# Kernel optimization log

Measured on AMD Instinct MI355X. Metric: run time of the kernel, lower is better.

## Reference

```python
import jax, jax.numpy as jnp
import numpy as np

T, HQ, HKV, D, R = 2048, 16, 4, 128, 8
NEG = -1e30


def apply_rope(x, cos, sin):
    # x: [T, H, D]; cos/sin: [T, D//2]; non-interleaved rotary over full head dim
    c = jnp.concatenate([cos, cos], axis=-1)[:, None, :]  # [T,1,D]
    s = jnp.concatenate([sin, sin], axis=-1)[:, None, :]
    half = x.shape[-1] // 2
    x1, x2 = x[..., :half], x[..., half:]
    rot = jnp.concatenate([-x2, x1], axis=-1)
    return x * c + rot * s


def setup_inputs() -> dict:
    key = jax.random.key(0)
    kq, kk, kv = jax.random.split(key, 3)
    q = jax.random.normal(kq, (T, HQ, D), dtype=jnp.float32)
    k = jax.random.normal(kk, (T, HKV, D), dtype=jnp.float32)
    v = jax.random.normal(kv, (T, HKV, D), dtype=jnp.float32)
    # standard rotary tables
    inv_freq = 1.0 / (10000.0 ** (np.arange(0, D, 2, dtype=np.float32) / D))
    ang = np.arange(T, dtype=np.float32)[:, None] * inv_freq[None, :]  # [T, D/2]
    cos = jnp.asarray(np.cos(ang), dtype=jnp.float32)
    sin = jnp.asarray(np.sin(ang), dtype=jnp.float32)
    # block-causal ranges: q block r attends to keys [0, (r+1)*B)
    B = T // R
    q_ranges = jnp.asarray([[r * B, (r + 1) * B] for r in range(R)], dtype=jnp.int32)
    k_ranges = jnp.asarray([[0, (r + 1) * B] for r in range(R)], dtype=jnp.int32)
    return {"q": q, "k": k, "v": v, "cos": cos, "sin": sin,
            "q_ranges": q_ranges, "k_ranges": k_ranges}


def reference(q, k, v, cos, sin, q_ranges, k_ranges):
    scale = 1.0 / jnp.sqrt(jnp.float32(D))
    qh = apply_rope(q, cos, sin)
    kh = apply_rope(k, cos, sin)
    rep = HQ // HKV
    kr = jnp.repeat(kh, rep, axis=1)  # [T,HQ,D]
    vr = jnp.repeat(v, rep, axis=1)
    idx = jnp.arange(T)
    qm = (idx[None, :] >= q_ranges[:, :1]) & (idx[None, :] < q_ranges[:, 1:])  # [R,T]
    km = (idx[None, :] >= k_ranges[:, :1]) & (idx[None, :] < k_ranges[:, 1:])  # [R,T]
    mask = jnp.any(qm[:, :, None] & km[:, None, :], axis=0)  # [T,T] union over ranges
    scores = jnp.einsum('qhd,khd->hqk', qh, kr) * scale  # [HQ,T,T]
    scores = jnp.where(mask[None], scores, NEG)
    p = jax.nn.softmax(scores, axis=-1)
    row_valid = jnp.any(mask, axis=-1)  # [T]
    p = jnp.where(row_valid[None, :, None], p, 0.0)  # uncovered q rows output zero
    out = jnp.einsum('hqk,khd->qhd', p, vr)
    return out
```

## Files before the change

### kernel.cpp

```cpp
#include <hip/hip_runtime.h>
#include <hip/hip_bf16.h>

#define T_   2048
#define HQ_  16
#define HKV_ 4
#define D_   128
#define QBLK 64
#define NQB  (T_/QBLK)
#define KVBLK 64

typedef float f32x4 __attribute__((ext_vector_type(4)));
typedef __bf16 bf16x8 __attribute__((ext_vector_type(8)));
typedef unsigned short u16;
typedef unsigned short u16x8 __attribute__((ext_vector_type(8)));
typedef unsigned long long u64;

__device__ __forceinline__ u16 f2bf(float f) {
  unsigned u = __builtin_bit_cast(unsigned, f);
  u += 0x7FFFu + ((u >> 16) & 1u);
  return (u16)(u >> 16);
}

#define QK_BLOCKS 1280
__global__ __launch_bounds__(256) void prep_all(
    const float* __restrict__ q, const float* __restrict__ k,
    const float* __restrict__ v, const float* __restrict__ ct,
    const float* __restrict__ st,
    u16* __restrict__ qr, u16* __restrict__ kr, u16* __restrict__ vt)
{
  __shared__ __attribute__((aligned(16))) char Lv[32 * 144];
  const int tid = threadIdx.x;
  const int bid = blockIdx.x;
  if (bid < QK_BLOCKS) {
    const float scale = 0.08838834764831845f;
    const int NQT = T_ * HQ_ * 8;
    int gid = bid * 256 + tid;
    if (gid < NQT) {
      int j0 = (gid & 7) * 8;
      int h  = (gid >> 3) & 15;
      int t  = gid >> 7;
      const float* base = q + ((size_t)t * HQ_ + h) * D_;
      const float* cb = ct + t * 64 + j0;
      const float* sb = st + t * 64 + j0;
      u16 lo[8], hi[8];
#pragma unroll
      for (int e = 0; e < 8; ++e) {
        float x1 = base[j0 + e], x2 = base[j0 + 64 + e];
        float c = cb[e], s = sb[e];
        lo[e] = f2bf((x1 * c - x2 * s) * scale);
        hi[e] = f2bf((x2 * c + x1 * s) * scale);
      }
      u16* orow = qr + ((size_t)h * T_ + t) * D_;
      *reinterpret_cast<u16x8*>(orow + j0)      = *reinterpret_cast<u16x8*>(lo);
      *reinterpret_cast<u16x8*>(orow + 64 + j0) = *reinterpret_cast<u16x8*>(hi);
    } else {
      int th = gid - NQT;
      int j0 = (th & 7) * 8;
      int hh = (th >> 3) & 3;
      int t  = th >> 5;
      const float* base = k + ((size_t)t * HKV_ + hh) * D_;
      const float* cb = ct + t * 64 + j0;
      const float* sb = st + t * 64 + j0;
      u16 lo[8], hi[8];
#pragma unroll
      for (int e = 0; e < 8; ++e) {
        float x1 = base[j0 + e], x2 = base[j0 + 64 + e];
        float c = cb[e], s = sb[e];
        lo[e] = f2bf(x1 * c - x2 * s);
        hi[e] = f2bf(x2 * c + x1 * s);
      }
      u16* orow = kr + ((size_t)hh * T_ + t) * D_;
      *reinterpret_cast<u16x8*>(orow + j0)      = *reinterpret_cast<u16x8*>(lo);
      *reinterpret_cast<u16x8*>(orow + 64 + j0) = *reinterpret_cast<u16x8*>(hi);
    }
  } else {
    int vbid = bid - QK_BLOCKS;
    int hh = vbid & 3;
    int t0 = ((vbid >> 2) & 31) * 64;
    int d0 = (vbid >> 7) * 32;
    {
      int r  = tid >> 2;
      int dg = tid & 3;
      const float* vrow = v + ((size_t)(t0 + r) * HKV_ + hh) * D_ + d0 + dg * 8;
      float4 f0 = *reinterpret_cast<const float4*>(vrow);
      float4 f1 = *reinterpret_cast<const float4*>(vrow + 4);
      float fv[8] = {f0.x, f0.y, f0.z, f0.w, f1.x, f1.y, f1.z, f1.w};
#pragma unroll
      for (int e = 0; e < 8; ++e)
        *reinterpret_cast<u16*>(Lv + (dg * 8 + e) * 144 + r * 2) = f2bf(fv[e]);
    }
    __syncthreads();
    {
      int dl = tid >> 3;
      int c0 = (tid & 7) * 16;
      u16x8 val = *reinterpret_cast<const u16x8*>(Lv + dl * 144 + c0);
      u16* orow = vt + ((size_t)(hh * D_ + d0 + dl)) * T_ + t0 + (c0 >> 1);
      *reinterpret_cast<u16x8*>(orow) = val;
    }
  }
}

__global__ __launch_bounds__(256, 2) void attn_fwd(
    const u16* __restrict__ qr, const u16* __restrict__ kr,
    const u16* __restrict__ vt, float* __restrict__ out)
{
  __shared__ __attribute__((aligned(16))) char lds[73728];

  const int tid  = threadIdx.x;
  const int lane = tid & 63;
  const int wv   = tid >> 6;
  char* Plds = lds + 65536 + wv * 2048;

  const int bid = blockIdx.x;
  const int qb  = (NQB - 1) - (bid >> 4);
  const int h   = bid & 15;
  const int hkv = h >> 2;
  const int q0  = qb * QBLK + wv * 16;
  const int nt  = ((qb >> 2) + 1) * 4;

  const int lm = lane & 15;
  const int lh = lane >> 4;

  bf16x8 qf[4];
  {
    const u16* qrow = qr + ((size_t)h * T_ + q0 + lm) * D_;
#pragma unroll
    for (int kb = 0; kb < 4; ++kb)
      qf[kb] = *reinterpret_cast<const bf16x8*>(qrow + kb * 32 + lh * 8);
  }

  const u16* kbase = kr + (size_t)hkv * T_ * D_;
  const u16* vbase = vt + (size_t)hkv * D_ * T_;

  bf16x8 kpf[4], vpf[4];
#pragma unroll
  for (int j = 0; j < 4; ++j) {
    kpf[j] = *reinterpret_cast<const bf16x8*>(kbase + j * 2048 + tid * 8);
    int d = j * 32 + (tid >> 3);
    vpf[j] = *reinterpret_cast<const bf16x8*>(vbase + (size_t)d * T_ + (tid & 7) * 8);
  }

  f32x4 accO[8];
#pragma unroll
  for (int c = 0; c < 8; ++c) accO[c] = (f32x4){0.f, 0.f, 0.f, 0.f};
  float mrun = -1e30f, lrun = 0.f;

  for (int t = 0; t < nt; ++t) {
    char* Klds  = lds + (t & 1) * 16384;
    char* VTlds = lds + 32768 + (t & 1) * 16384;
#pragma unroll
    for (int j = 0; j < 4; ++j) {
      int off = j * 4096 + tid * 16;
      int row = off >> 8;
      *reinterpret_cast<bf16x8*>(Klds + (off ^ ((row & 7) << 4))) = kpf[j];
      int d = j * 32 + (tid >> 3);
      int offv = d * 128 + (tid & 7) * 16;
      *reinterpret_cast<bf16x8*>(VTlds + (offv ^ ((d & 7) << 4))) = vpf[j];
    }
    if (t + 1 < nt) {
      const u16* kb2 = kbase + (size_t)(t + 1) * KVBLK * D_;
      const u16* vb2 = vbase + (size_t)(t + 1) * KVBLK;
#pragma unroll
      for (int j = 0; j < 4; ++j) {
        kpf[j] = *reinterpret_cast<const bf16x8*>(kb2 + j * 2048 + tid * 8);
        int d = j * 32 + (tid >> 3);
        vpf[j] = *reinterpret_cast<const bf16x8*>(vb2 + (size_t)d * T_ + (tid & 7) * 8);
      }
    }
    __syncthreads();

    f32x4 s[4];
#pragma unroll
    for (int g = 0; g < 4; ++g) s[g] = (f32x4){0.f, 0.f, 0.f, 0.f};
    __builtin_amdgcn_s_setprio(1);
#pragma unroll
    for (int kb = 0; kb < 4; ++kb) {
#pragma unroll
      for (int g = 0; g < 4; ++g) {
        int row = lm + 16 * g;
        bf16x8 kf = *reinterpret_cast<const bf16x8*>(
            Klds + ((row * 256 + kb * 64 + lh * 16) ^ ((row & 7) << 4)));
        s[g] = __builtin_amdgcn_mfma_f32_16x16x32_bf16(kf, qf[kb], s[g], 0, 0, 0);
      }
    }
    __builtin_amdgcn_s_setprio(0);

    float tmax = -1e30f;
#pragma unroll
    for (int g = 0; g < 4; ++g)
      tmax = fmaxf(tmax, fmaxf(fmaxf(s[g][0], s[g][1]), fmaxf(s[g][2], s[g][3])));
    tmax = fmaxf(tmax, __shfl_xor(tmax, 16));
    tmax = fmaxf(tmax, __shfl_xor(tmax, 32));
    float mnew  = fmaxf(mrun, tmax);
    float alpha = __expf(mrun - mnew);
    float psum = 0.f;
#pragma unroll
    for (int g = 0; g < 4; ++g) {
      float p0 = __expf(s[g][0] - mnew), p1 = __expf(s[g][1] - mnew);
      float p2 = __expf(s[g][2] - mnew), p3 = __expf(s[g][3] - mnew);
      psum += (p0 + p1) + (p2 + p3);
      u64 w = (u64)f2bf(p0) | ((u64)f2bf(p1) << 16) |
              ((u64)f2bf(p2) << 32) | ((u64)f2bf(p3) << 48);
      *reinterpret_cast<u64*>(
          Plds + lm * 128 + ((g * 32 + lh * 8) ^ ((lm & 7) << 4))) = w;
    }
    psum += __shfl_xor(psum, 16);
    psum += __shfl_xor(psum, 32);
    lrun = lrun * alpha + psum;
    mrun = mnew;
#pragma unroll
    for (int c = 0; c < 8; ++c) {
      accO[c][0] *= alpha; accO[c][1] *= alpha;
      accO[c][2] *= alpha; accO[c][3] *= alpha;
    }

    bf16x8 pf[2];
#pragma unroll
    for (int half = 0; half < 2; ++half)
      pf[half] = *reinterpret_cast<const bf16x8*>(
          Plds + lm * 128 + ((half * 64 + lh * 16) ^ ((lm & 7) << 4)));
    __builtin_amdgcn_s_setprio(1);
#pragma unroll
    for (int c = 0; c < 8; ++c) {
#pragma unroll
      for (int half = 0; half < 2; ++half) {
        int row = c * 16 + lm;
        bf16x8 vf = *reinterpret_cast<const bf16x8*>(
            VTlds + ((row * 128 + half * 64 + lh * 16) ^ ((row & 7) << 4)));
        accO[c] = __builtin_amdgcn_mfma_f32_16x16x32_bf16(vf, pf[half], accO[c], 0, 0, 0);
      }
    }
    __builtin_amdgcn_s_setprio(0);
  }

  float inv = 1.f / lrun;
  float* orow = out + ((size_t)(q0 + lm) * HQ_ + h) * D_ + lh * 4;
#pragma unroll
  for (int c = 0; c < 8; ++c) {
    f32x4 o;
    o[0] = accO[c][0] * inv; o[1] = accO[c][1] * inv;
    o[2] = accO[c][2] * inv; o[3] = accO[c][3] * inv;
    *reinterpret_cast<f32x4*>(orow + c * 16) = o;
  }
}

extern "C" void kernel_launch(void* const* d_in, const int* in_sizes, int n_in,
                              void* d_out, int out_size, void* d_ws, size_t ws_size,
                              hipStream_t stream) {
  const float* q  = (const float*)d_in[0];
  const float* k  = (const float*)d_in[1];
  const float* v  = (const float*)d_in[2];
  const float* ct = (const float*)d_in[3];
  const float* st = (const float*)d_in[4];

  u16* qr = (u16*)d_ws;
  u16* kr = qr + (size_t)T_ * HQ_ * D_;
  u16* vt = kr + (size_t)T_ * HKV_ * D_;
  float* out = (float*)d_out;

  prep_all<<<QK_BLOCKS + 512, 256, 0, stream>>>(q, k, v, ct, st, qr, kr, vt);
  attn_fwd<<<NQB * HQ_, 256, 0, stream>>>(qr, kr, vt, out);
}
```

Baseline: 133.0 us.

## Software-pipeline PV MFMA into next iteration, remap block schedule, use packed bf16 convert

Defers each tile's P·V MFMAs to the start of the next iteration, issuing them alongside the Q·K MFMAs so softmax work can overlap matrix-core work. The V fragments are held in 16 registers across iterations. The block-to-(head, q-block) mapping is changed to interleave long and short causal q-blocks, aiming for better load balance across CUs. The manual bf16 rounding is replaced with the v_cvt_pk_bf16_f32 instruction. The extra live registers risk spills or lower occupancy under the 2-block launch bound.

```diff
diff --git a/kernel.cpp b/kernel.cpp
--- a/kernel.cpp
+++ b/kernel.cpp
@@ -14,6 +14,7 @@
 typedef unsigned short u16;
 typedef unsigned short u16x8 __attribute__((ext_vector_type(8)));
 typedef unsigned long long u64;
+typedef unsigned u32;
 
 __device__ __forceinline__ u16 f2bf(float f) {
   unsigned u = __builtin_bit_cast(unsigned, f);
@@ -112,8 +113,10 @@
   char* Plds = lds + 65536 + wv * 2048;
 
   const int bid = blockIdx.x;
-  const int qb  = (NQB - 1) - (bid >> 4);
-  const int h   = bid & 15;
+  const int f   = (bid ^ (bid >> 8)) & 1;
+  const int x   = (bid >> 4) & 15;
+  const int h   = ((bid >> 1) & 7) | (((bid >> 8) & 1) << 3);
+  const int qb  = f ? (31 - x) : x;
   const int hkv = h >> 2;
   const int q0  = qb * QBLK + wv * 16;
   const int nt  = ((qb >> 2) + 1) * 4;
@@ -132,18 +135,28 @@
   const u16* kbase = kr + (size_t)hkv * T_ * D_;
   const u16* vbase = vt + (size_t)hkv * D_ * T_;
 
-  bf16x8 kpf[4], vpf[4];
+  bf16x8 ksta[4], vsta[4];
 #pragma unroll
   for (int j = 0; j < 4; ++j) {
-    kpf[j] = *reinterpret_cast<const bf16x8*>(kbase + j * 2048 + tid * 8);
+    ksta[j] = *reinterpret_cast<const bf16x8*>(kbase + j * 2048 + tid * 8);
     int d = j * 32 + (tid >> 3);
-    vpf[j] = *reinterpret_cast<const bf16x8*>(vbase + (size_t)d * T_ + (tid & 7) * 8);
+    vsta[j] = *reinterpret_cast<const bf16x8*>(vbase + (size_t)d * T_ + (tid & 7) * 8);
   }
 
   f32x4 accO[8];
 #pragma unroll
   for (int c = 0; c < 8; ++c) accO[c] = (f32x4){0.f, 0.f, 0.f, 0.f};
   float mrun = -1e30f, lrun = 0.f;
+
+  bf16x8 vf[16], pf[2];
+#pragma unroll
+  for (int i = 0; i < 16; ++i)
+#pragma unroll
+    for (int e = 0; e < 8; ++e) vf[i][e] = (__bf16)0.f;
+#pragma unroll
+  for (int i = 0; i < 2; ++i)
+#pragma unroll
+    for (int e = 0; e < 8; ++e) pf[i][e] = (__bf16)0.f;
 
   for (int t = 0; t < nt; ++t) {
     char* Klds  = lds + (t & 1) * 16384;
@@ -152,19 +165,19 @@
     for (int j = 0; j < 4; ++j) {
       int off = j * 4096 + tid * 16;
       int row = off >> 8;
-      *reinterpret_cast<bf16x8*>(Klds + (off ^ ((row & 7) << 4))) = kpf[j];
+      *reinterpret_cast<bf16x8*>(Klds + (off ^ ((row & 7) << 4))) = ksta[j];
       int d = j * 32 + (tid >> 3);
       int offv = d * 128 + (tid & 7) * 16;
-      *reinterpret_cast<bf16x8*>(VTlds + (offv ^ ((d & 7) << 4))) = vpf[j];
+      *reinterpret_cast<bf16x8*>(VTlds + (offv ^ ((d & 7) << 4))) = vsta[j];
     }
     if (t + 1 < nt) {
       const u16* kb2 = kbase + (size_t)(t + 1) * KVBLK * D_;
       const u16* vb2 = vbase + (size_t)(t + 1) * KVBLK;
 #pragma unroll
       for (int j = 0; j < 4; ++j) {
-        kpf[j] = *reinterpret_cast<const bf16x8*>(kb2 + j * 2048 + tid * 8);
+        ksta[j] = *reinterpret_cast<const bf16x8*>(kb2 + j * 2048 + tid * 8);
         int d = j * 32 + (tid >> 3);
-        vpf[j] = *reinterpret_cast<const bf16x8*>(vb2 + (size_t)d * T_ + (tid & 7) * 8);
+        vsta[j] = *reinterpret_cast<const bf16x8*>(vb2 + (size_t)d * T_ + (tid & 7) * 8);
       }
     }
     __syncthreads();
@@ -173,6 +186,11 @@
 #pragma unroll
     for (int g = 0; g < 4; ++g) s[g] = (f32x4){0.f, 0.f, 0.f, 0.f};
     __builtin_amdgcn_s_setprio(1);
+#pragma unroll
+    for (int c = 0; c < 8; ++c) {
+      accO[c] = __builtin_amdgcn_mfma_f32_16x16x32_bf16(vf[2*c],   pf[0], accO[c], 0, 0, 0);
+      accO[c] = __builtin_amdgcn_mfma_f32_16x16x32_bf16(vf[2*c+1], pf[1], accO[c], 0, 0, 0);
+    }
 #pragma unroll
     for (int kb = 0; kb < 4; ++kb) {
 #pragma unroll
@@ -184,6 +202,15 @@
       }
     }
     __builtin_amdgcn_s_setprio(0);
+
+#pragma unroll
+    for (int c = 0; c < 8; ++c)
+#pragma unroll
+      for (int half = 0; half < 2; ++half) {
+        int row = c * 16 + lm;
+        vf[2*c + half] = *reinterpret_cast<const bf16x8*>(
+            VTlds + ((row * 128 + half * 64 + lh * 16) ^ ((row & 7) << 4)));
+      }
 
     float tmax = -1e30f;
 #pragma unroll
@@ -199,8 +226,10 @@
       float p0 = __expf(s[g][0] - mnew), p1 = __expf(s[g][1] - mnew);
       float p2 = __expf(s[g][2] - mnew), p3 = __expf(s[g][3] - mnew);
       psum += (p0 + p1) + (p2 + p3);
-      u64 w = (u64)f2bf(p0) | ((u64)f2bf(p1) << 16) |
-              ((u64)f2bf(p2) << 32) | ((u64)f2bf(p3) << 48);
+      u32 r01, r23;
+      asm("v_cvt_pk_bf16_f32 %0, %1, %2" : "=v"(r01) : "v"(p0), "v"(p1));
+      asm("v_cvt_pk_bf16_f32 %0, %1, %2" : "=v"(r23) : "v"(p2), "v"(p3));
+      u64 w = (u64)r01 | ((u64)r23 << 32);
       *reinterpret_cast<u64*>(
           Plds + lm * 128 + ((g * 32 + lh * 8) ^ ((lm & 7) << 4))) = w;
     }
@@ -213,25 +242,19 @@
       accO[c][0] *= alpha; accO[c][1] *= alpha;
       accO[c][2] *= alpha; accO[c][3] *= alpha;
     }
-
-    bf16x8 pf[2];
 #pragma unroll
     for (int half = 0; half < 2; ++half)
       pf[half] = *reinterpret_cast<const bf16x8*>(
           Plds + lm * 128 + ((half * 64 + lh * 16) ^ ((lm & 7) << 4)));
-    __builtin_amdgcn_s_setprio(1);
-#pragma unroll
-    for (int c = 0; c < 8; ++c) {
-#pragma unroll
-      for (int half = 0; half < 2; ++half) {
-        int row = c * 16 + lm;
-        bf16x8 vf = *reinterpret_cast<const bf16x8*>(
-            VTlds + ((row * 128 + half * 64 + lh * 16) ^ ((row & 7) << 4)));
-        accO[c] = __builtin_amdgcn_mfma_f32_16x16x32_bf16(vf, pf[half], accO[c], 0, 0, 0);
-      }
-    }
-    __builtin_amdgcn_s_setprio(0);
-  }
+  }
+
+  __builtin_amdgcn_s_setprio(1);
+#pragma unroll
+  for (int c = 0; c < 8; ++c) {
+    accO[c] = __builtin_amdgcn_mfma_f32_16x16x32_bf16(vf[2*c],   pf[0], accO[c], 0, 0, 0);
+    accO[c] = __builtin_amdgcn_mfma_f32_16x16x32_bf16(vf[2*c+1], pf[1], accO[c], 0, 0, 0);
+  }
+  __builtin_amdgcn_s_setprio(0);
 
   float inv = 1.f / lrun;
   float* orow = out + ((size_t)(q0 + lm) * HQ_ + h) * D_ + lh * 4;
```

Result: faster. 129.8 us (-2.4%).

## Halve KV tile to raise occupancy, remap blocks, use packed bf16 convert

Applied to the files above, without the earlier changes.

Shrinks the KV tile from 64 to 32 keys, which cuts LDS from 72KB to 40KB and lets launch bounds request 4 blocks per CU instead of 2. The V-transpose LDS layout is repacked so two d-rows share a 128-byte row with an XOR swizzle. Block-to-(head, q-block) mapping is changed to interleave long and short causal rows and balance the load. The softmax probabilities are packed with the v_cvt_pk_bf16_f32 instruction. In exchange it doubles the loop trip count, so there are twice as many barriers and softmax reductions per key processed.

```diff
diff --git a/kernel.cpp b/kernel.cpp
--- a/kernel.cpp
+++ b/kernel.cpp
@@ -7,13 +7,14 @@
 #define D_   128
 #define QBLK 64
 #define NQB  (T_/QBLK)
-#define KVBLK 64
+#define KVBLK 32
 
 typedef float f32x4 __attribute__((ext_vector_type(4)));
 typedef __bf16 bf16x8 __attribute__((ext_vector_type(8)));
 typedef unsigned short u16;
 typedef unsigned short u16x8 __attribute__((ext_vector_type(8)));
 typedef unsigned long long u64;
+typedef unsigned u32;
 
 __device__ __forceinline__ u16 f2bf(float f) {
   unsigned u = __builtin_bit_cast(unsigned, f);
@@ -100,23 +101,25 @@
   }
 }
 
-__global__ __launch_bounds__(256, 2) void attn_fwd(
+__global__ __launch_bounds__(256, 4) void attn_fwd(
     const u16* __restrict__ qr, const u16* __restrict__ kr,
     const u16* __restrict__ vt, float* __restrict__ out)
 {
-  __shared__ __attribute__((aligned(16))) char lds[73728];
+  __shared__ __attribute__((aligned(16))) char lds[40960];
 
   const int tid  = threadIdx.x;
   const int lane = tid & 63;
   const int wv   = tid >> 6;
-  char* Plds = lds + 65536 + wv * 2048;
+  char* Plds = lds + 32768 + wv * 2048;
 
   const int bid = blockIdx.x;
-  const int qb  = (NQB - 1) - (bid >> 4);
-  const int h   = bid & 15;
+  const int f   = (bid ^ (bid >> 8)) & 1;
+  const int x   = (bid >> 4) & 15;
+  const int h   = ((bid >> 1) & 7) | (((bid >> 8) & 1) << 3);
+  const int qb  = f ? (31 - x) : x;
   const int hkv = h >> 2;
   const int q0  = qb * QBLK + wv * 16;
-  const int nt  = ((qb >> 2) + 1) * 4;
+  const int nt  = ((qb >> 2) + 1) * 8;
 
   const int lm = lane & 15;
   const int lh = lane >> 4;
@@ -132,12 +135,18 @@
   const u16* kbase = kr + (size_t)hkv * T_ * D_;
   const u16* vbase = vt + (size_t)hkv * D_ * T_;
 
-  bf16x8 kpf[4], vpf[4];
-#pragma unroll
-  for (int j = 0; j < 4; ++j) {
-    kpf[j] = *reinterpret_cast<const bf16x8*>(kbase + j * 2048 + tid * 8);
-    int d = j * 32 + (tid >> 3);
-    vpf[j] = *reinterpret_cast<const bf16x8*>(vbase + (size_t)d * T_ + (tid & 7) * 8);
+  const int ks_row  = tid >> 4;
+  const int ks_colb = (tid & 15) * 16;
+  const int vs_d    = tid >> 1;
+  const int vs_half = tid & 1;
+
+  bf16x8 ksta[2], vsta[2];
+#pragma unroll
+  for (int j = 0; j < 2; ++j) {
+    ksta[j] = *reinterpret_cast<const bf16x8*>(
+        kbase + (size_t)(ks_row + j * 16) * D_ + (ks_colb >> 1));
+    vsta[j] = *reinterpret_cast<const bf16x8*>(
+        vbase + (size_t)vs_d * T_ + vs_half * 16 + j * 8);
   }
 
   f32x4 accO[8];
@@ -146,37 +155,38 @@
   float mrun = -1e30f, lrun = 0.f;
 
   for (int t = 0; t < nt; ++t) {
-    char* Klds  = lds + (t & 1) * 16384;
-    char* VTlds = lds + 32768 + (t & 1) * 16384;
-#pragma unroll
-    for (int j = 0; j < 4; ++j) {
-      int off = j * 4096 + tid * 16;
-      int row = off >> 8;
-      *reinterpret_cast<bf16x8*>(Klds + (off ^ ((row & 7) << 4))) = kpf[j];
-      int d = j * 32 + (tid >> 3);
-      int offv = d * 128 + (tid & 7) * 16;
-      *reinterpret_cast<bf16x8*>(VTlds + (offv ^ ((d & 7) << 4))) = vpf[j];
+    char* Klds  = lds + (t & 1) * 8192;
+    char* VTlds = lds + 16384 + (t & 1) * 8192;
+#pragma unroll
+    for (int j = 0; j < 2; ++j) {
+      int row = ks_row + j * 16;
+      int off = row * 256 + ks_colb;
+      *reinterpret_cast<bf16x8*>(Klds + (off ^ ((row & 7) << 4))) = ksta[j];
+      int prow = vs_d >> 1;
+      int colb = (vs_d & 1) * 64 + vs_half * 32 + j * 16;
+      *reinterpret_cast<bf16x8*>(
+          VTlds + prow * 128 + (colb ^ ((prow & 7) << 4))) = vsta[j];
     }
     if (t + 1 < nt) {
-      const u16* kb2 = kbase + (size_t)(t + 1) * KVBLK * D_;
-      const u16* vb2 = vbase + (size_t)(t + 1) * KVBLK;
-#pragma unroll
-      for (int j = 0; j < 4; ++j) {
-        kpf[j] = *reinterpret_cast<const bf16x8*>(kb2 + j * 2048 + tid * 8);
-        int d = j * 32 + (tid >> 3);
-        vpf[j] = *reinterpret_cast<const bf16x8*>(vb2 + (size_t)d * T_ + (tid & 7) * 8);
+      const int kv1 = (t + 1) * KVBLK;
+#pragma unroll
+      for (int j = 0; j < 2; ++j) {
+        ksta[j] = *reinterpret_cast<const bf16x8*>(
+            kbase + (size_t)(kv1 + ks_row + j * 16) * D_ + (ks_colb >> 1));
+        vsta[j] = *reinterpret_cast<const bf16x8*>(
+            vbase + (size_t)vs_d * T_ + kv1 + vs_half * 16 + j * 8);
       }
     }
     __syncthreads();
 
-    f32x4 s[4];
-#pragma unroll
-    for (int g = 0; g < 4; ++g) s[g] = (f32x4){0.f, 0.f, 0.f, 0.f};
+    f32x4 s[2];
+#pragma unroll
+    for (int g = 0; g < 2; ++g) s[g] = (f32x4){0.f, 0.f, 0.f, 0.f};
     __builtin_amdgcn_s_setprio(1);
 #pragma unroll
     for (int kb = 0; kb < 4; ++kb) {
 #pragma unroll
-      for (int g = 0; g < 4; ++g) {
+      for (int g = 0; g < 2; ++g) {
         int row = lm + 16 * g;
         bf16x8 kf = *reinterpret_cast<const bf16x8*>(
             Klds + ((row * 256 + kb * 64 + lh * 16) ^ ((row & 7) << 4)));
@@ -185,22 +195,22 @@
     }
     __builtin_amdgcn_s_setprio(0);
 
-    float tmax = -1e30f;
-#pragma unroll
-    for (int g = 0; g < 4; ++g)
-      tmax = fmaxf(tmax, fmaxf(fmaxf(s[g][0], s[g][1]), fmaxf(s[g][2], s[g][3])));
+    float tmax = fmaxf(fmaxf(fmaxf(s[0][0], s[0][1]), fmaxf(s[0][2], s[0][3])),
+                       fmaxf(fmaxf(s[1][0], s[1][1]), fmaxf(s[1][2], s[1][3])));
     tmax = fmaxf(tmax, __shfl_xor(tmax, 16));
     tmax = fmaxf(tmax, __shfl_xor(tmax, 32));
     float mnew  = fmaxf(mrun, tmax);
     float alpha = __expf(mrun - mnew);
     float psum = 0.f;
 #pragma unroll
-    for (int g = 0; g < 4; ++g) {
+    for (int g = 0; g < 2; ++g) {
       float p0 = __expf(s[g][0] - mnew), p1 = __expf(s[g][1] - mnew);
       float p2 = __expf(s[g][2] - mnew), p3 = __expf(s[g][3] - mnew);
       psum += (p0 + p1) + (p2 + p3);
-      u64 w = (u64)f2bf(p0) | ((u64)f2bf(p1) << 16) |
-              ((u64)f2bf(p2) << 32) | ((u64)f2bf(p3) << 48);
+      u32 r01, r23;
+      asm("v_cvt_pk_bf16_f32 %0, %1, %2" : "=v"(r01) : "v"(p0), "v"(p1));
+      asm("v_cvt_pk_bf16_f32 %0, %1, %2" : "=v"(r23) : "v"(p2), "v"(p3));
+      u64 w = (u64)r01 | ((u64)r23 << 32);
       *reinterpret_cast<u64*>(
           Plds + lm * 128 + ((g * 32 + lh * 8) ^ ((lm & 7) << 4))) = w;
     }
@@ -214,21 +224,17 @@
       accO[c][2] *= alpha; accO[c][3] *= alpha;
     }
 
-    bf16x8 pf[2];
-#pragma unroll
-    for (int half = 0; half < 2; ++half)
-      pf[half] = *reinterpret_cast<const bf16x8*>(
-          Plds + lm * 128 + ((half * 64 + lh * 16) ^ ((lm & 7) << 4)));
+    bf16x8 pf = *reinterpret_cast<const bf16x8*>(
+        Plds + lm * 128 + ((lh * 16) ^ ((lm & 7) << 4)));
     __builtin_amdgcn_s_setprio(1);
 #pragma unroll
     for (int c = 0; c < 8; ++c) {
-#pragma unroll
-      for (int half = 0; half < 2; ++half) {
-        int row = c * 16 + lm;
-        bf16x8 vf = *reinterpret_cast<const bf16x8*>(
-            VTlds + ((row * 128 + half * 64 + lh * 16) ^ ((row & 7) << 4)));
-        accO[c] = __builtin_amdgcn_mfma_f32_16x16x32_bf16(vf, pf[half], accO[c], 0, 0, 0);
-      }
+      int row  = c * 16 + lm;
+      int prow = row >> 1;
+      int colb = (row & 1) * 64 + lh * 16;
+      bf16x8 vf = *reinterpret_cast<const bf16x8*>(
+          VTlds + prow * 128 + (colb ^ ((prow & 7) << 4)));
+      accO[c] = __builtin_amdgcn_mfma_f32_16x16x32_bf16(vf, pf, accO[c], 0, 0, 0);
     }
     __builtin_amdgcn_s_setprio(0);
   }
```

Measured after the change: 134.0 us. Within noise of the previous version (+0.8%).

## Split attention into single-wave KV-chunk partials with a separate combine kernel

Applied to the files above, without the earlier changes.

Replaces the 256-thread, LDS-staged flash-attention kernel with 4608 single-wave blocks. Each block handles one 32-row query tile against one 256-key chunk, reading K and V straight from global memory into registers and using 32x32x16 MFMAs. The P fragment is built with a lane shuffle instead of an LDS round trip. Partial outputs are stored in bf16 with per-row max and sum, and a new reduce kernel merges them with log-sum-exp weights. The aim is to fix load imbalance across the block-causal triangle and drop LDS traffic and barriers, at the cost of an extra launch, partial-result memory traffic, and bf16 rounding of the partials.

```diff
diff --git a/kernel.cpp b/kernel.cpp
--- a/kernel.cpp
+++ b/kernel.cpp
@@ -5,20 +5,23 @@
 #define HQ_  16
 #define HKV_ 4
 #define D_   128
-#define QBLK 64
-#define NQB  (T_/QBLK)
-#define KVBLK 64
-
-typedef float f32x4 __attribute__((ext_vector_type(4)));
+
+typedef float f32x4  __attribute__((ext_vector_type(4)));
+typedef float f32x16 __attribute__((ext_vector_type(16)));
 typedef __bf16 bf16x8 __attribute__((ext_vector_type(8)));
 typedef unsigned short u16;
 typedef unsigned short u16x8 __attribute__((ext_vector_type(8)));
+typedef unsigned int u32;
+typedef u32 u32x4 __attribute__((ext_vector_type(4)));
 typedef unsigned long long u64;
 
 __device__ __forceinline__ u16 f2bf(float f) {
-  unsigned u = __builtin_bit_cast(unsigned, f);
+  u32 u = __builtin_bit_cast(u32, f);
   u += 0x7FFFu + ((u >> 16) & 1u);
   return (u16)(u >> 16);
+}
+__device__ __forceinline__ float bf2f(u16 v) {
+  return __builtin_bit_cast(float, (u32)v << 16);
 }
 
 #define QK_BLOCKS 1280
@@ -100,147 +103,184 @@
   }
 }
 
-__global__ __launch_bounds__(256, 2) void attn_fwd(
+__global__ __launch_bounds__(64, 2) void attn_fwd(
     const u16* __restrict__ qr, const u16* __restrict__ kr,
-    const u16* __restrict__ vt, float* __restrict__ out)
+    const u16* __restrict__ vt, u32* __restrict__ part,
+    float* __restrict__ stats)
 {
-  __shared__ __attribute__((aligned(16))) char lds[73728];
-
-  const int tid  = threadIdx.x;
-  const int lane = tid & 63;
-  const int wv   = tid >> 6;
-  char* Plds = lds + 65536 + wv * 2048;
+  const int lane = threadIdx.x;
+  const int ql = lane & 31;
+  const int hi = lane >> 5;
 
   const int bid = blockIdx.x;
-  const int qb  = (NQB - 1) - (bid >> 4);
-  const int h   = bid & 15;
-  const int hkv = h >> 2;
-  const int q0  = qb * QBLK + wv * 16;
-  const int nt  = ((qb >> 2) + 1) * 4;
-
-  const int lm = lane & 15;
-  const int lh = lane >> 4;
-
-  bf16x8 qf[4];
+  const int slot = (bid & 7) * 576 + (bid >> 3);
+  const int hkv = slot / 1152;
+  const int r1  = slot - hkv * 1152;
+  const int pair = r1 >> 2, hl = r1 & 3;
+  int g = 0;
+  while (4 * (g + 1) * (g + 2) <= pair) ++g;
+  const int cb = g + 1;
+  const int r  = pair - 4 * g * (g + 1);
+  const int qq = r / cb, ck = r - qq * cb;
+  const int qb32 = 8 * g + qq;
+  const int h  = hkv * 4 + hl;
+  const int q0 = qb32 * 32;
+  const int kvb = ck * 256;
+
+  bf16x8 qf[8];
   {
-    const u16* qrow = qr + ((size_t)h * T_ + q0 + lm) * D_;
-#pragma unroll
-    for (int kb = 0; kb < 4; ++kb)
-      qf[kb] = *reinterpret_cast<const bf16x8*>(qrow + kb * 32 + lh * 8);
-  }
-
-  const u16* kbase = kr + (size_t)hkv * T_ * D_;
-  const u16* vbase = vt + (size_t)hkv * D_ * T_;
-
-  bf16x8 kpf[4], vpf[4];
-#pragma unroll
-  for (int j = 0; j < 4; ++j) {
-    kpf[j] = *reinterpret_cast<const bf16x8*>(kbase + j * 2048 + tid * 8);
-    int d = j * 32 + (tid >> 3);
-    vpf[j] = *reinterpret_cast<const bf16x8*>(vbase + (size_t)d * T_ + (tid & 7) * 8);
-  }
-
-  f32x4 accO[8];
-#pragma unroll
-  for (int c = 0; c < 8; ++c) accO[c] = (f32x4){0.f, 0.f, 0.f, 0.f};
+    const u16* qrow = qr + ((size_t)h * T_ + q0 + ql) * D_ + hi * 8;
+#pragma unroll
+    for (int kb = 0; kb < 8; ++kb)
+      qf[kb] = *reinterpret_cast<const bf16x8*>(qrow + kb * 16);
+  }
+
+  const u16* krow = kr + ((size_t)hkv * T_ + kvb + ql) * D_ + hi * 8;
+  const u16* vrow = vt + ((size_t)hkv * D_ + ql) * T_ + kvb + hi * 8;
+
+  f32x16 accO[4] = {};
   float mrun = -1e30f, lrun = 0.f;
 
-  for (int t = 0; t < nt; ++t) {
-    char* Klds  = lds + (t & 1) * 16384;
-    char* VTlds = lds + 32768 + (t & 1) * 16384;
-#pragma unroll
-    for (int j = 0; j < 4; ++j) {
-      int off = j * 4096 + tid * 16;
-      int row = off >> 8;
-      *reinterpret_cast<bf16x8*>(Klds + (off ^ ((row & 7) << 4))) = kpf[j];
-      int d = j * 32 + (tid >> 3);
-      int offv = d * 128 + (tid & 7) * 16;
-      *reinterpret_cast<bf16x8*>(VTlds + (offv ^ ((d & 7) << 4))) = vpf[j];
-    }
-    if (t + 1 < nt) {
-      const u16* kb2 = kbase + (size_t)(t + 1) * KVBLK * D_;
-      const u16* vb2 = vbase + (size_t)(t + 1) * KVBLK;
-#pragma unroll
-      for (int j = 0; j < 4; ++j) {
-        kpf[j] = *reinterpret_cast<const bf16x8*>(kb2 + j * 2048 + tid * 8);
-        int d = j * 32 + (tid >> 3);
-        vpf[j] = *reinterpret_cast<const bf16x8*>(vb2 + (size_t)d * T_ + (tid & 7) * 8);
-      }
-    }
-    __syncthreads();
-
-    f32x4 s[4];
-#pragma unroll
-    for (int g = 0; g < 4; ++g) s[g] = (f32x4){0.f, 0.f, 0.f, 0.f};
+#pragma unroll
+  for (int t = 0; t < 8; ++t) {
+    const u16* kt = krow + (size_t)t * 32 * D_;
+    bf16x8 kf[8];
+#pragma unroll
+    for (int kb = 0; kb < 8; ++kb)
+      kf[kb] = *reinterpret_cast<const bf16x8*>(kt + kb * 16);
+    bf16x8 vf[8];
+#pragma unroll
+    for (int c = 0; c < 4; ++c)
+#pragma unroll
+      for (int hf = 0; hf < 2; ++hf)
+        vf[c * 2 + hf] = *reinterpret_cast<const bf16x8*>(
+            vrow + (size_t)c * 32 * T_ + t * 32 + hf * 16);
+
+    f32x16 s = {};
     __builtin_amdgcn_s_setprio(1);
 #pragma unroll
-    for (int kb = 0; kb < 4; ++kb) {
-#pragma unroll
-      for (int g = 0; g < 4; ++g) {
-        int row = lm + 16 * g;
-        bf16x8 kf = *reinterpret_cast<const bf16x8*>(
-            Klds + ((row * 256 + kb * 64 + lh * 16) ^ ((row & 7) << 4)));
-        s[g] = __builtin_amdgcn_mfma_f32_16x16x32_bf16(kf, qf[kb], s[g], 0, 0, 0);
-      }
-    }
+    for (int kb = 0; kb < 8; ++kb)
+      s = __builtin_amdgcn_mfma_f32_32x32x16_bf16(kf[kb], qf[kb], s, 0, 0, 0);
     __builtin_amdgcn_s_setprio(0);
 
-    float tmax = -1e30f;
-#pragma unroll
-    for (int g = 0; g < 4; ++g)
-      tmax = fmaxf(tmax, fmaxf(fmaxf(s[g][0], s[g][1]), fmaxf(s[g][2], s[g][3])));
-    tmax = fmaxf(tmax, __shfl_xor(tmax, 16));
+    float t0m = fmaxf(fmaxf(fmaxf(s[0], s[1]), fmaxf(s[2], s[3])),
+                      fmaxf(fmaxf(s[4], s[5]), fmaxf(s[6], s[7])));
+    float t1m = fmaxf(fmaxf(fmaxf(s[8], s[9]), fmaxf(s[10], s[11])),
+                      fmaxf(fmaxf(s[12], s[13]), fmaxf(s[14], s[15])));
+    float tmax = fmaxf(t0m, t1m);
     tmax = fmaxf(tmax, __shfl_xor(tmax, 32));
     float mnew  = fmaxf(mrun, tmax);
     float alpha = __expf(mrun - mnew);
+    float p[16];
     float psum = 0.f;
 #pragma unroll
-    for (int g = 0; g < 4; ++g) {
-      float p0 = __expf(s[g][0] - mnew), p1 = __expf(s[g][1] - mnew);
-      float p2 = __expf(s[g][2] - mnew), p3 = __expf(s[g][3] - mnew);
-      psum += (p0 + p1) + (p2 + p3);
-      u64 w = (u64)f2bf(p0) | ((u64)f2bf(p1) << 16) |
-              ((u64)f2bf(p2) << 32) | ((u64)f2bf(p3) << 48);
-      *reinterpret_cast<u64*>(
-          Plds + lm * 128 + ((g * 32 + lh * 8) ^ ((lm & 7) << 4))) = w;
-    }
-    psum += __shfl_xor(psum, 16);
+    for (int i = 0; i < 16; ++i) { p[i] = __expf(s[i] - mnew); psum += p[i]; }
     psum += __shfl_xor(psum, 32);
     lrun = lrun * alpha + psum;
     mrun = mnew;
 #pragma unroll
-    for (int c = 0; c < 8; ++c) {
-      accO[c][0] *= alpha; accO[c][1] *= alpha;
-      accO[c][2] *= alpha; accO[c][3] *= alpha;
-    }
-
-    bf16x8 pf[2];
-#pragma unroll
-    for (int half = 0; half < 2; ++half)
-      pf[half] = *reinterpret_cast<const bf16x8*>(
-          Plds + lm * 128 + ((half * 64 + lh * 16) ^ ((lm & 7) << 4)));
+    for (int c = 0; c < 4; ++c)
+#pragma unroll
+      for (int i = 0; i < 16; ++i) accO[c][i] *= alpha;
+
+    u32 P[8], X[8];
+#pragma unroll
+    for (int j = 0; j < 8; ++j) {
+      u32 w;
+      asm("v_cvt_pk_bf16_f32 %0, %1, %2" : "=v"(w) : "v"(p[2 * j]), "v"(p[2 * j + 1]));
+      P[j] = w;
+    }
+#pragma unroll
+    for (int j = 0; j < 8; ++j) X[j] = (u32)__shfl_xor((int)P[j], 32);
+    u32x4 f0 = { hi ? X[2] : P[0], hi ? X[3] : P[1],
+                 hi ? P[2] : X[0], hi ? P[3] : X[1] };
+    u32x4 f1 = { hi ? X[6] : P[4], hi ? X[7] : P[5],
+                 hi ? P[6] : X[4], hi ? P[7] : X[5] };
+    bf16x8 pf0 = __builtin_bit_cast(bf16x8, f0);
+    bf16x8 pf1 = __builtin_bit_cast(bf16x8, f1);
+
     __builtin_amdgcn_s_setprio(1);
 #pragma unroll
-    for (int c = 0; c < 8; ++c) {
-#pragma unroll
-      for (int half = 0; half < 2; ++half) {
-        int row = c * 16 + lm;
-        bf16x8 vf = *reinterpret_cast<const bf16x8*>(
-            VTlds + ((row * 128 + half * 64 + lh * 16) ^ ((row & 7) << 4)));
-        accO[c] = __builtin_amdgcn_mfma_f32_16x16x32_bf16(vf, pf[half], accO[c], 0, 0, 0);
+    for (int c = 0; c < 4; ++c) {
+      accO[c] = __builtin_amdgcn_mfma_f32_32x32x16_bf16(vf[c * 2],     pf0, accO[c], 0, 0, 0);
+      accO[c] = __builtin_amdgcn_mfma_f32_32x32x16_bf16(vf[c * 2 + 1], pf1, accO[c], 0, 0, 0);
+    }
+    __builtin_amdgcn_s_setprio(0);
+  }
+
+  u32* pp = part + (size_t)slot * 2048;
+#pragma unroll
+  for (int c = 0; c < 4; ++c)
+#pragma unroll
+    for (int j = 0; j < 8; ++j) {
+      u32 w;
+      asm("v_cvt_pk_bf16_f32 %0, %1, %2"
+          : "=v"(w) : "v"(accO[c][2 * j]), "v"(accO[c][2 * j + 1]));
+      int dp = c * 16 + (j & 1) + 4 * (j >> 1) + 2 * hi;
+      pp[dp * 32 + ql] = w;
+    }
+  if (hi == 0) {
+    float2 ml = make_float2(mrun, lrun);
+    *reinterpret_cast<float2*>(stats + (size_t)slot * 64 + ql * 2) = ml;
+  }
+}
+
+__global__ __launch_bounds__(256) void reduce_k(
+    const u32* __restrict__ part, const float* __restrict__ stats,
+    float* __restrict__ out)
+{
+  const int bid  = blockIdx.x;
+  const int qb32 = bid >> 4;
+  const int h    = bid & 15;
+  const int hkv  = h >> 2, hl = h & 3;
+  const int g    = qb32 >> 3, qq = qb32 & 7;
+  const int cb   = g + 1;
+  const int pairbase = 4 * g * (g + 1) + qq * cb;
+
+  const int t  = threadIdx.x;
+  const int q  = t & 31;
+  const int dg = t >> 5;
+
+  float m[8], l[8];
+  float M = -1e30f;
+#pragma unroll
+  for (int ck = 0; ck < 8; ++ck)
+    if (ck < cb) {
+      int slot = hkv * 1152 + (pairbase + ck) * 4 + hl;
+      float2 ml = *reinterpret_cast<const float2*>(stats + (size_t)slot * 64 + q * 2);
+      m[ck] = ml.x; l[ck] = ml.y;
+      M = fmaxf(M, m[ck]);
+    }
+  float L = 0.f, w[8];
+#pragma unroll
+  for (int ck = 0; ck < 8; ++ck)
+    if (ck < cb) { w[ck] = __expf(m[ck] - M); L += w[ck] * l[ck]; }
+  float inv = 1.f / L;
+
+  float acc[16];
+#pragma unroll
+  for (int e = 0; e < 16; ++e) acc[e] = 0.f;
+#pragma unroll
+  for (int ck = 0; ck < 8; ++ck)
+    if (ck < cb) {
+      int slot = hkv * 1152 + (pairbase + ck) * 4 + hl;
+      const u32* pp = part + (size_t)slot * 2048 + dg * 256 + q;
+      float wc = w[ck];
+#pragma unroll
+      for (int j = 0; j < 8; ++j) {
+        u32 v = pp[j * 32];
+        acc[2 * j]     += wc * bf2f((u16)(v & 0xFFFF));
+        acc[2 * j + 1] += wc * bf2f((u16)(v >> 16));
       }
     }
-    __builtin_amdgcn_s_setprio(0);
-  }
-
-  float inv = 1.f / lrun;
-  float* orow = out + ((size_t)(q0 + lm) * HQ_ + h) * D_ + lh * 4;
-#pragma unroll
-  for (int c = 0; c < 8; ++c) {
+
+  float* orow = out + ((size_t)(qb32 * 32 + q) * HQ_ + h) * D_ + dg * 16;
+#pragma unroll
+  for (int j = 0; j < 4; ++j) {
     f32x4 o;
-    o[0] = accO[c][0] * inv; o[1] = accO[c][1] * inv;
-    o[2] = accO[c][2] * inv; o[3] = accO[c][3] * inv;
-    *reinterpret_cast<f32x4*>(orow + c * 16) = o;
+    o[0] = acc[4 * j + 0] * inv; o[1] = acc[4 * j + 1] * inv;
+    o[2] = acc[4 * j + 2] * inv; o[3] = acc[4 * j + 3] * inv;
+    *reinterpret_cast<f32x4*>(orow + 4 * j) = o;
   }
 }
 
@@ -256,8 +296,11 @@
   u16* qr = (u16*)d_ws;
   u16* kr = qr + (size_t)T_ * HQ_ * D_;
   u16* vt = kr + (size_t)T_ * HKV_ * D_;
+  u32* part = (u32*)(vt + (size_t)T_ * HKV_ * D_);
+  float* stats = (float*)(part + (size_t)4608 * 2048);
   float* out = (float*)d_out;
 
   prep_all<<<QK_BLOCKS + 512, 256, 0, stream>>>(q, k, v, ct, st, qr, kr, vt);
-  attn_fwd<<<NQB * HQ_, 256, 0, stream>>>(qr, kr, vt, out);
-}
+  attn_fwd<<<4608, 64, 0, stream>>>(qr, kr, vt, part, stats);
+  reduce_k<<<1024, 256, 0, stream>>>(part, stats, out);
+}
```

Result: slower. 174.0 us (+30.8%).
